# Kernel tuning notes

Measured on AMD Instinct MI355X. Metric: run time of the kernel, lower is better.

Reference implementation:

```python
import jax, jax.numpy as jnp
import numpy as np

N, E, R = 50000, 800000, 8
EMB, PROJ, H, OUT = 512, 256, 256, 200


def rgcn_conv(x, src, dst, rel, W, root, bias):
    # PyG RGCNConv: per-relation linear transform, mean aggregation per relation
    # over incoming edges, summed across relations, plus root transform + bias.
    n = x.shape[0]
    r, _, out_dim = W.shape
    h = jnp.einsum('ni,rio->nro', x, W)            # [N,R,out] per-relation transforms
    msgs = h[src, rel]                             # [E,out] gather per-edge messages
    seg = dst * r + rel                            # combined (node, relation) segment id
    sums = jax.ops.segment_sum(msgs, seg, num_segments=n * r)
    cnt = jax.ops.segment_sum(jnp.ones((src.shape[0],), x.dtype), seg, num_segments=n * r)
    mean = sums / jnp.maximum(cnt, 1.0)[:, None]
    agg = mean.reshape(n, r, out_dim).sum(axis=1)  # sum over relations
    return agg + x @ root + bias


def setup_inputs() -> dict:
    key = jax.random.key(0)
    ks = jax.random.split(key, 16)
    inp = {
        'embeddings': jax.random.normal(ks[0], (N, EMB), jnp.float32),
        'node_indices': jnp.arange(N, dtype=jnp.int64) if jax.config.jax_enable_x64 else jnp.arange(N, dtype=jnp.int32),
        'src': jax.random.randint(ks[1], (E,), 0, N),
        'dst': jax.random.randint(ks[2], (E,), 0, N),
        'rel': jax.random.randint(ks[3], (E,), 0, R),
        'neg_src': jax.random.randint(ks[4], (E,), 0, N),
        'neg_dst': jax.random.randint(ks[5], (E,), 0, N),
        'neg_rel': jax.random.randint(ks[6], (E,), 0, R),
        # learned parameters
        'Wp': jax.random.normal(ks[7], (EMB, PROJ), jnp.float32) * 0.04,
        'bp': jnp.zeros((PROJ,), jnp.float32),
        'W0': jax.random.normal(ks[8], (R, PROJ, H), jnp.float32) * 0.06,
        'root0': jax.random.normal(ks[9], (PROJ, H), jnp.float32) * 0.06,
        'b0': jnp.zeros((H,), jnp.float32),
        'W1': jax.random.normal(ks[10], (R, H, H), jnp.float32) * 0.06,
        'root1': jax.random.normal(ks[11], (H, H), jnp.float32) * 0.06,
        'b1': jnp.zeros((H,), jnp.float32),
        'W2': jax.random.normal(ks[12], (R, H, OUT), jnp.float32) * 0.06,
        'root2': jax.random.normal(ks[13], (H, OUT), jnp.float32) * 0.06,
        'b2': jnp.zeros((OUT,), jnp.float32),
        'rel_emb': jax.random.normal(ks[14], (R, OUT), jnp.float32),
    }
    return inp


def reference(embeddings, node_indices, src, dst, rel, neg_src, neg_dst, neg_rel,
              Wp, bp, W0, root0, b0, W1, root1, b1, W2, root2, b2, rel_emb):
    # projection: Linear per modality, then reorder rows by node index (sort)
    proj = embeddings @ Wp + bp                        # [N,PROJ]
    x = jnp.zeros_like(proj).at[node_indices].set(proj)
    # stacked RGCN encoder with relu between layers (no relu on last)
    x = jax.nn.relu(rgcn_conv(x, src, dst, rel, W0, root0, b0))
    x = jax.nn.relu(rgcn_conv(x, src, dst, rel, W1, root1, b1))
    out = rgcn_conv(x, src, dst, rel, W2, root2, b2)   # [N,OUT]
    # DistMult decoder over positive + negative triples
    s = jnp.concatenate([src, neg_src])
    o = jnp.concatenate([dst, neg_dst])
    r = jnp.concatenate([rel, neg_rel])
    scores = jnp.sum(out[s] * rel_emb[r] * out[o], axis=-1)  # [2E]
    return out, scores
```

## Files before the change

kernel.cpp:

```cpp
#include <hip/hip_runtime.h>
#include <stdint.h>

#define NN 50000
#define NE 800000
#define NR 8
#define EMBD 512
#define PROJD 256
#define HIDD 256
#define OUTD 200
#define NSEG (NN * NR)
#define CSR_CAP 1536

typedef _Float16 half8 __attribute__((ext_vector_type(8)));
typedef _Float16 half4 __attribute__((ext_vector_type(4)));
typedef float f32x4 __attribute__((ext_vector_type(4)));

__device__ __forceinline__ void gload16(const void* g, void* l) {
    __builtin_amdgcn_global_load_lds(
        reinterpret_cast<const __attribute__((address_space(1))) uint32_t*>(
            reinterpret_cast<uintptr_t>(g)),
        reinterpret_cast<__attribute__((address_space(3))) uint32_t*>(
            reinterpret_cast<uintptr_t>(l)),
        16, 0, 0);
}


__global__ void count_edges(const int* __restrict__ dst, const int* __restrict__ rel,
                            int* __restrict__ cnt, int E) {
    int e = blockIdx.x * 256 + threadIdx.x;
    if (e >= E) return;
    atomicAdd(&cnt[dst[e] * NR + rel[e]], 1);
}

__global__ __launch_bounds__(512) void scan1(const int* __restrict__ cnt, int* __restrict__ offs,
                                             int* __restrict__ bsums, int n) {
    __shared__ int sm[512];
    int tid = threadIdx.x;
    int g = blockIdx.x * 512 + tid;
    int v = (g < n) ? cnt[g] : 0;
    sm[tid] = v;
    __syncthreads();
    for (int o = 1; o < 512; o <<= 1) {
        int t = (tid >= o) ? sm[tid - o] : 0;
        __syncthreads();
        sm[tid] += t;
        __syncthreads();
    }
    if (g < n) offs[g] = sm[tid] - v;
    if (tid == 511) bsums[blockIdx.x] = sm[511];
}

__global__ __launch_bounds__(1024) void scan2(const int* __restrict__ bsums, int* __restrict__ bpref, int nb) {
    __shared__ int sm[1024];
    int tid = threadIdx.x;
    int v = (tid < nb) ? bsums[tid] : 0;
    sm[tid] = v;
    __syncthreads();
    for (int o = 1; o < 1024; o <<= 1) {
        int t = (tid >= o) ? sm[tid - o] : 0;
        __syncthreads();
        sm[tid] += t;
        __syncthreads();
    }
    if (tid < nb) bpref[tid] = sm[tid] - v;
}

__global__ __launch_bounds__(512) void scan3(int* __restrict__ offs, int* __restrict__ cursor,
                                             const int* __restrict__ bpref, int n, int total) {
    int g = blockIdx.x * 512 + threadIdx.x;
    if (g < n) {
        int v = offs[g] + bpref[blockIdx.x];
        offs[g] = v;
        cursor[g] = v;
    }
    if (g == 0) offs[n] = total;
}

__global__ void pad_offs(int* __restrict__ offs, int total) {
    offs[NSEG + 1 + blockIdx.x * 256 + threadIdx.x] = total;
}

__global__ void scatter_edges(const int* __restrict__ dst, const int* __restrict__ rel,
                              const int* __restrict__ src, int* __restrict__ cursor,
                              int* __restrict__ csr, int E) {
    int e = blockIdx.x * 256 + threadIdx.x;
    if (e >= E) return;
    int seg = dst[e] * NR + rel[e];
    int pos = atomicAdd(&cursor[seg], 1);
    csr[pos] = src[e];
}


__global__ void f32_to_f16_vec(const float* __restrict__ in, _Float16* __restrict__ out, long n4) {
    long i = (long)blockIdx.x * 256 + threadIdx.x;
    long stride = (long)gridDim.x * 256;
    for (; i < n4; i += stride) {
        float4 v = ((const float4*)in)[i];
        half4 h;
        h[0] = (_Float16)v.x; h[1] = (_Float16)v.y; h[2] = (_Float16)v.z; h[3] = (_Float16)v.w;
        ((half4*)out)[i] = h;
    }
}

__global__ void build_bt(const float* __restrict__ S0, int K0, const float* __restrict__ S1,
                         _Float16* __restrict__ Bt, int N, int K) {
    int k = blockIdx.x * 256 + threadIdx.x;
    int n = blockIdx.y;
    if (k >= K) return;
    float v = (k < K0) ? S0[(size_t)k * N + n] : S1[(size_t)(k - K0) * N + n];
    Bt[(size_t)n * K + k] = (_Float16)v;
}


template <bool RELU, bool LAST>
__global__ __launch_bounds__(512, 4) void rgcn_layer(
    const _Float16* __restrict__ x, const _Float16* __restrict__ Bt,
    const int* __restrict__ csr, const int* __restrict__ offs,
    const float* __restrict__ bias,
    _Float16* __restrict__ C16, int ldc, float* __restrict__ C32, int N) {
    __shared__ _Float16 As[64 * 256];
    __shared__ _Float16 Bs[2][256 * 32];
    __shared__ int offs_lds[520];
    __shared__ int csr_lds[CSR_CAP];
    const int tid = threadIdx.x;
    const int lane = tid & 63, wave = tid >> 6;
    const int lane32 = tid & 31, hw = tid >> 5;
    const int half_base = lane & 32;
    const int l15 = lane & 15, q = lane >> 4;
    const int wm = wave >> 2, wn = wave & 3;
    const int m0 = blockIdx.x * 64;
    const int segbase = m0 * NR;

    for (int i = tid; i < 513; i += 512) offs_lds[i] = offs[segbase + i];
    __syncthreads();
    const int e0 = offs_lds[0];
    const int e1 = offs_lds[512];
    const int ecnt = min(e1 - e0, CSR_CAP);
    for (int i = tid; i < ecnt; i += 512) csr_lds[i] = csr[e0 + i];
    __syncthreads();

    auto stage = [&](int buf, int g) {
        int kbase = g * 32;
#pragma unroll
        for (int h = 0; h < 2; ++h) {
            int s = tid + h * 512;
            int n = s >> 2, c4 = s & 3;
            int nn = n < N ? n : N - 1;
            gload16(Bt + (size_t)nn * 2304 + kbase + ((c4 ^ (n & 3)) << 3),
                    &Bs[buf][(size_t)(wave * 64 + h * 512) * 8]);
        }
    };

    f32x4 acc[2][4] = {};
    stage(0, 0);
    int cur = 0;
    for (int seg = 0; seg < 9; ++seg) {
#pragma unroll
        for (int u = 0; u < 4; ++u) {
            int lr = u * 16 + hw;
            int nd = m0 + lr;
            if (nd >= NN) nd = NN - 1;
            half8 hv;
            if (seg == 0) {
                hv = *(const half8*)(x + (size_t)nd * 256 + lane32 * 8);
            } else {
                int sb = lr * NR + seg - 1;
                int o0 = offs_lds[sb], o1 = offs_lds[sb + 1];
                int n = o1 - o0;
                if (n < 0) n = 0;
                if (n == 0) {
#pragma unroll
                    for (int z = 0; z < 8; ++z) hv[z] = (_Float16)0.f;
                } else {
                    bool staged = (o1 - e0) <= CSR_CAP;
                    int fi = o0 + (lane32 < n ? lane32 : n - 1);
                    int idxv = staged ? csr_lds[fi - e0] : csr[fi];
                    float a0=0.f,a1=0.f,a2=0.f,a3=0.f,a4=0.f,a5=0.f,a6=0.f,a7=0.f;
                    int nb = n < 32 ? n : 32;
                    int e = 0;
                    for (; e + 4 <= nb; e += 4) {
                        int s0 = __shfl(idxv, half_base + e);
                        int s1 = __shfl(idxv, half_base + e + 1);
                        int s2 = __shfl(idxv, half_base + e + 2);
                        int s3 = __shfl(idxv, half_base + e + 3);
                        half8 v0 = *(const half8*)(x + (size_t)s0 * 256 + lane32 * 8);
                        half8 v1 = *(const half8*)(x + (size_t)s1 * 256 + lane32 * 8);
                        half8 v2 = *(const half8*)(x + (size_t)s2 * 256 + lane32 * 8);
                        half8 v3 = *(const half8*)(x + (size_t)s3 * 256 + lane32 * 8);
                        a0 += ((float)v0[0] + (float)v1[0]) + ((float)v2[0] + (float)v3[0]);
                        a1 += ((float)v0[1] + (float)v1[1]) + ((float)v2[1] + (float)v3[1]);
                        a2 += ((float)v0[2] + (float)v1[2]) + ((float)v2[2] + (float)v3[2]);
                        a3 += ((float)v0[3] + (float)v1[3]) + ((float)v2[3] + (float)v3[3]);
                        a4 += ((float)v0[4] + (float)v1[4]) + ((float)v2[4] + (float)v3[4]);
                        a5 += ((float)v0[5] + (float)v1[5]) + ((float)v2[5] + (float)v3[5]);
                        a6 += ((float)v0[6] + (float)v1[6]) + ((float)v2[6] + (float)v3[6]);
                        a7 += ((float)v0[7] + (float)v1[7]) + ((float)v2[7] + (float)v3[7]);
                    }
                    for (; e < nb; ++e) {
                        int s0 = __shfl(idxv, half_base + e);
                        half8 v0 = *(const half8*)(x + (size_t)s0 * 256 + lane32 * 8);
                        a0 += (float)v0[0]; a1 += (float)v0[1];
                        a2 += (float)v0[2]; a3 += (float)v0[3];
                        a4 += (float)v0[4]; a5 += (float)v0[5];
                        a6 += (float)v0[6]; a7 += (float)v0[7];
                    }
                    for (int e2 = 32; e2 < n; ++e2) {
                        int s2i = staged ? csr_lds[o0 - e0 + e2] : csr[o0 + e2];
                        half8 v = *(const half8*)(x + (size_t)s2i * 256 + lane32 * 8);
                        a0 += (float)v[0]; a1 += (float)v[1];
                        a2 += (float)v[2]; a3 += (float)v[3];
                        a4 += (float)v[4]; a5 += (float)v[5];
                        a6 += (float)v[6]; a7 += (float)v[7];
                    }
                    float inv = 1.0f / (float)n;
                    hv[0] = (_Float16)(a0 * inv); hv[1] = (_Float16)(a1 * inv);
                    hv[2] = (_Float16)(a2 * inv); hv[3] = (_Float16)(a3 * inv);
                    hv[4] = (_Float16)(a4 * inv); hv[5] = (_Float16)(a5 * inv);
                    hv[6] = (_Float16)(a6 * inv); hv[7] = (_Float16)(a7 * inv);
                }
            }
            *(half8*)((char*)As + lr * 512 + ((lane32 ^ (lr & 31)) << 4)) = hv;
        }
        asm volatile("s_waitcnt lgkmcnt(0)" ::: "memory");
        __builtin_amdgcn_s_barrier();
        asm volatile("" ::: "memory");
        for (int ch = 0; ch < 8; ++ch) {
            int g = seg * 8 + ch;
            if (g < 71) {
                stage(cur ^ 1, g + 1);
                asm volatile("s_waitcnt vmcnt(2)" ::: "memory");
            } else {
                asm volatile("s_waitcnt vmcnt(0)" ::: "memory");
            }
            __builtin_amdgcn_s_barrier();
            asm volatile("" ::: "memory");
            half8 a[2], b[4];
#pragma unroll
            for (int i = 0; i < 2; ++i) {
                int row = wm * 32 + i * 16 + l15;
                int ck = ch * 4 + q;
                a[i] = *(const half8*)((const char*)As + row * 512 + ((ck ^ (row & 31)) << 4));
            }
#pragma unroll
            for (int j = 0; j < 4; ++j) {
                int n = wn * 64 + j * 16 + l15;
                b[j] = *(const half8*)((const char*)&Bs[cur][0] + n * 64 + ((q ^ (n & 3)) << 4));
            }
#pragma unroll
            for (int i = 0; i < 2; ++i)
#pragma unroll
                for (int j = 0; j < 4; ++j)
                    acc[i][j] = __builtin_amdgcn_mfma_f32_16x16x32_f16(a[i], b[j], acc[i][j], 0, 0, 0);
            asm volatile("s_waitcnt lgkmcnt(0)" ::: "memory");
            __builtin_amdgcn_s_barrier();
            asm volatile("" ::: "memory");
            cur ^= 1;
        }
    }
#pragma unroll
    for (int i = 0; i < 2; ++i) {
        int rbase = m0 + wm * 32 + i * 16 + q * 4;
#pragma unroll
        for (int j = 0; j < 4; ++j) {
            int cc = wn * 64 + j * 16 + l15;
            if (cc >= N) continue;
            float bv = bias[cc];
#pragma unroll
            for (int t = 0; t < 4; ++t) {
                int rr = rbase + t;
                if (rr >= NN) continue;
                float v = acc[i][j][t] + bv;
                if (RELU) v = fmaxf(v, 0.f);
                C16[(size_t)rr * ldc + cc] = (_Float16)v;
                if (LAST) C32[(size_t)rr * ldc + cc] = v;
            }
        }
    }
}


template <bool BIAS, bool ACC_IN, bool FINAL, bool RELU, bool LAST, bool SCATTER>
__global__ __launch_bounds__(256) void gemm16(
    const _Float16* __restrict__ A, int lda,
    const _Float16* __restrict__ Bt, int ldb,
    const float* __restrict__ bias, const int* __restrict__ sidx,
    _Float16* __restrict__ Cacc,
    _Float16* __restrict__ C16, int ldc, float* __restrict__ C32,
    int M, int N, int K) {
    __shared__ _Float16 As[2][4096];
    __shared__ _Float16 Bs[2][4096];
    const int tid = threadIdx.x;
    const int lane = tid & 63, wave = tid >> 6;
    const int wm = wave >> 1, wn = wave & 1;
    const int q = lane >> 4, l15 = lane & 15;
    const int m0 = blockIdx.y * 128, n0 = blockIdx.x * 128;
    const int wbase = wave * 512;
    f32x4 acc[4][4] = {};

    auto stage = [&](int buf, int k0) {
#pragma unroll
        for (int h = 0; h < 2; ++h) {
            int s = tid + h * 256;
            int r = s >> 2, c = s & 3;
            int cs = c ^ ((r >> 2) & 3);
            int ga = m0 + r; if (ga >= M) ga = M - 1;
            gload16(A + (size_t)ga * lda + k0 + cs * 8, &As[buf][wbase + h * 2048]);
            int gb = n0 + r; if (gb >= N) gb = N - 1;
            gload16(Bt + (size_t)gb * ldb + k0 + cs * 8, &Bs[buf][wbase + h * 2048]);
        }
    };

    const int nk = K >> 5;
    stage(0, 0);
    int cur = 0;
    for (int kt = 0; kt < nk; ++kt) {
        if (kt + 1 < nk) {
            stage(cur ^ 1, (kt + 1) << 5);
            asm volatile("s_waitcnt vmcnt(4)" ::: "memory");
        } else {
            asm volatile("s_waitcnt vmcnt(0)" ::: "memory");
        }
        __builtin_amdgcn_s_barrier();
        asm volatile("" ::: "memory");
        half8 a[4], b[4];
#pragma unroll
        for (int i = 0; i < 4; ++i) {
            int row = wm * 64 + i * 16 + l15;
            a[i] = *(const half8*)&As[cur][row * 32 + ((q ^ ((row >> 2) & 3)) << 3)];
            int col = wn * 64 + i * 16 + l15;
            b[i] = *(const half8*)&Bs[cur][col * 32 + ((q ^ ((col >> 2) & 3)) << 3)];
        }
#pragma unroll
        for (int i = 0; i < 4; ++i)
#pragma unroll
            for (int j = 0; j < 4; ++j)
                acc[i][j] = __builtin_amdgcn_mfma_f32_16x16x32_f16(a[i], b[j], acc[i][j], 0, 0, 0);
        asm volatile("s_waitcnt lgkmcnt(0)" ::: "memory");
        __builtin_amdgcn_s_barrier();
        asm volatile("" ::: "memory");
        cur ^= 1;
    }
#pragma unroll
    for (int i = 0; i < 4; ++i) {
        int rbase = m0 + wm * 64 + i * 16 + q * 4;
#pragma unroll
        for (int j = 0; j < 4; ++j) {
            int cc = n0 + wn * 64 + j * 16 + l15;
            if (cc >= N) continue;
#pragma unroll
            for (int t = 0; t < 4; ++t) {
                int rr = rbase + t;
                if (rr >= M) continue;
                float v = acc[i][j][t];
                if (BIAS) v += bias[cc];
                if (ACC_IN) v += (float)Cacc[(size_t)rr * 256 + cc];
                if (!FINAL) {
                    Cacc[(size_t)rr * 256 + cc] = (_Float16)v;
                } else {
                    if (RELU) v = fmaxf(v, 0.f);
                    int ro = SCATTER ? sidx[rr] : rr;
                    C16[(size_t)ro * ldc + cc] = (_Float16)v;
                    if (LAST) C32[(size_t)ro * ldc + cc] = v;
                }
            }
        }
    }
}


__global__ __launch_bounds__(256) void decoder16(
    const _Float16* __restrict__ out16, const _Float16* __restrict__ rel16,
    const int* __restrict__ src, const int* __restrict__ dst, const int* __restrict__ rel,
    const int* __restrict__ nsrc, const int* __restrict__ ndst, const int* __restrict__ nrel,
    float* __restrict__ scores) {
    int gid = blockIdx.x * 256 + threadIdx.x;
    int t = gid >> 3, lq = gid & 7;
    if (t >= 2 * NE) return;
    int s, o, r;
    if (t < NE) { s = src[t]; o = dst[t]; r = rel[t]; }
    else { int u = t - NE; s = nsrc[u]; o = ndst[u]; r = nrel[u]; }
    const half8* ps = (const half8*)(out16 + (size_t)s * OUTD);
    const half8* po = (const half8*)(out16 + (size_t)o * OUTD);
    const half8* pr = (const half8*)(rel16 + (size_t)r * OUTD);
    half8 hacc0 = {}, hacc1 = {};
#pragma unroll
    for (int it = 0; it < 4; ++it) {
        int c = it * 8 + lq;
        if (c < 25) {
            half8 a = ps[c], b = pr[c], d = po[c];
            half8 p = a * b * d;
            if (it & 1) hacc1 += p; else hacc0 += p;
        }
    }
    float acc = 0.f;
#pragma unroll
    for (int u = 0; u < 8; ++u) acc += (float)hacc0[u] + (float)hacc1[u];
#pragma unroll
    for (int off = 4; off; off >>= 1) acc += __shfl_xor(acc, off);
    if (lq == 0) scores[t] = acc;
}


extern "C" void kernel_launch(void* const* d_in, const int* in_sizes, int n_in,
                              void* d_out, int out_size, void* d_ws, size_t ws_size,
                              hipStream_t stream) {
    const float* emb   = (const float*)d_in[0];
    const int*   nidx  = (const int*)d_in[1];
    const int*   src   = (const int*)d_in[2];
    const int*   dst   = (const int*)d_in[3];
    const int*   rel   = (const int*)d_in[4];
    const int*   nsrc  = (const int*)d_in[5];
    const int*   ndst  = (const int*)d_in[6];
    const int*   nrel  = (const int*)d_in[7];
    const float* Wp    = (const float*)d_in[8];
    const float* bp    = (const float*)d_in[9];
    const float* W0    = (const float*)d_in[10];
    const float* root0 = (const float*)d_in[11];
    const float* b0    = (const float*)d_in[12];
    const float* W1    = (const float*)d_in[13];
    const float* root1 = (const float*)d_in[14];
    const float* b1    = (const float*)d_in[15];
    const float* W2    = (const float*)d_in[16];
    const float* root2 = (const float*)d_in[17];
    const float* b2    = (const float*)d_in[18];
    const float* rele  = (const float*)d_in[19];
    (void)in_sizes; (void)n_in; (void)out_size; (void)ws_size;

    float* out    = (float*)d_out;
    float* scores = out + (size_t)NN * OUTD;

    auto align = [](size_t x) { return (x + 255) & ~(size_t)255; };
    char* p = (char*)d_ws;
    auto alloc = [&](size_t bytes) -> char* {
        char* q = p; p += align(bytes); return q;
    };
    _Float16* emb16  = (_Float16*)alloc((size_t)NN * EMBD * 2);
    _Float16* xbufA  = (_Float16*)alloc((size_t)NN * 256 * 2);
    _Float16* xbufB  = (_Float16*)alloc((size_t)NN * 256 * 2);
    _Float16* out16  = xbufB;
    _Float16* Bt0 = (_Float16*)alloc((size_t)256 * 2304 * 2);
    _Float16* Bt1 = (_Float16*)alloc((size_t)256 * 2304 * 2);
    _Float16* Bt2 = (_Float16*)alloc((size_t)256 * 2304 * 2);
    _Float16* BtP = (_Float16*)alloc((size_t)256 * EMBD * 2);
    _Float16* rel16 = (_Float16*)alloc((size_t)NR * OUTD * 2);
    int*   cnt    = (int*)alloc((size_t)NSEG * 4);
    int*   cursor = (int*)alloc((size_t)NSEG * 4);
    int*   offs   = (int*)alloc((size_t)(NSEG + 1032) * 4);
    int*   csr    = (int*)alloc((size_t)NE * 4);
    int*   bsums  = (int*)alloc(4096);
    int*   bpref  = (int*)alloc(4096);

    hipMemsetAsync(cnt, 0, (size_t)NSEG * 4, stream);
    count_edges<<<(NE + 255) / 256, 256, 0, stream>>>(dst, rel, cnt, NE);
    const int NB = (NSEG + 511) / 512;
    scan1<<<NB, 512, 0, stream>>>(cnt, offs, bsums, NSEG);
    scan2<<<1, 1024, 0, stream>>>(bsums, bpref, NB);
    scan3<<<NB, 512, 0, stream>>>(offs, cursor, bpref, NSEG, NE);
    pad_offs<<<4, 256, 0, stream>>>(offs, NE);
    scatter_edges<<<(NE + 255) / 256, 256, 0, stream>>>(dst, rel, src, cursor, csr, NE);

    f32_to_f16_vec<<<2048, 256, 0, stream>>>(emb, emb16, (long)NN * EMBD / 4);
    f32_to_f16_vec<<<2, 256, 0, stream>>>(rele, rel16, (long)NR * OUTD / 4);
    build_bt<<<dim3(2, 256), 256, 0, stream>>>(Wp, EMBD, nullptr, BtP, PROJD, EMBD);
    build_bt<<<dim3(9, 256), 256, 0, stream>>>(root0, 256, W0, Bt0, HIDD, 2304);
    build_bt<<<dim3(9, 256), 256, 0, stream>>>(root1, 256, W1, Bt1, HIDD, 2304);
    build_bt<<<dim3(9, 200), 256, 0, stream>>>(root2, 256, W2, Bt2, OUTD, 2304);

    {
        dim3 g(2, (NN + 127) / 128);
        gemm16<true, false, true, false, false, true><<<g, 256, 0, stream>>>(
            emb16, EMBD, BtP, EMBD, bp, nidx, nullptr, xbufA, 256, nullptr, NN, 256, EMBD);
    }

    const int GL = (NN + 63) / 64;
    rgcn_layer<true, false><<<GL, 512, 0, stream>>>(xbufA, Bt0, csr, offs, b0,
                                                    xbufB, 256, nullptr, HIDD);
    rgcn_layer<true, false><<<GL, 512, 0, stream>>>(xbufB, Bt1, csr, offs, b1,
                                                    xbufA, 256, nullptr, HIDD);
    rgcn_layer<false, true><<<GL, 512, 0, stream>>>(xbufA, Bt2, csr, offs, b2,
                                                    out16, OUTD, out, OUTD);

    decoder16<<<(2 * NE * 8 + 255) / 256, 256, 0, stream>>>(out16, rel16, src, dst, rel,
                                                            nsrc, ndst, nrel, scores);
}
```

Measured before the change: 883.0 us.

## Give each wave private B column slices to drop per-chunk barriers in RGCN layer

Re-partitions the rgcn_layer MFMA tiling so each of the 8 waves owns a 32-column slice of the output across all 64 rows and stages only its own B rows into LDS. Because no wave reads another wave's B data, the two workgroup barriers per K-chunk are removed, leaving one barrier per segment. It also fully unrolls the chunk loop and raises wave priority around the MFMA block. Each wave now reads all four A fragments per chunk, which increases LDS read traffic. Separately, the pad_offs launch is folded into scan3 by running extra blocks that write the padding totals.

```diff
diff --git a/kernel.cpp b/kernel.cpp
--- a/kernel.cpp
+++ b/kernel.cpp
@@ -72,12 +72,9 @@
         int v = offs[g] + bpref[blockIdx.x];
         offs[g] = v;
         cursor[g] = v;
-    }
-    if (g == 0) offs[n] = total;
-}
-
-__global__ void pad_offs(int* __restrict__ offs, int total) {
-    offs[NSEG + 1 + blockIdx.x * 256 + threadIdx.x] = total;
+    } else if (g <= n + 1024) {
+        offs[g] = total;
+    }
 }
 
 __global__ void scatter_edges(const int* __restrict__ dst, const int* __restrict__ rel,
@@ -127,7 +124,6 @@
     const int lane32 = tid & 31, hw = tid >> 5;
     const int half_base = lane & 32;
     const int l15 = lane & 15, q = lane >> 4;
-    const int wm = wave >> 2, wn = wave & 3;
     const int m0 = blockIdx.x * 64;
     const int segbase = m0 * NR;
 
@@ -143,15 +139,16 @@
         int kbase = g * 32;
 #pragma unroll
         for (int h = 0; h < 2; ++h) {
-            int s = tid + h * 512;
-            int n = s >> 2, c4 = s & 3;
+            int s = lane + h * 64;
+            int n = wave * 32 + (s >> 2);
+            int c4 = s & 3;
             int nn = n < N ? n : N - 1;
             gload16(Bt + (size_t)nn * 2304 + kbase + ((c4 ^ (n & 3)) << 3),
-                    &Bs[buf][(size_t)(wave * 64 + h * 512) * 8]);
+                    &Bs[buf][wave * 1024 + h * 512]);
         }
     };
 
-    f32x4 acc[2][4] = {};
+    f32x4 acc[4][2] = {};
     stage(0, 0);
     int cur = 0;
     for (int seg = 0; seg < 9; ++seg) {
@@ -224,6 +221,7 @@
         asm volatile("s_waitcnt lgkmcnt(0)" ::: "memory");
         __builtin_amdgcn_s_barrier();
         asm volatile("" ::: "memory");
+#pragma unroll
         for (int ch = 0; ch < 8; ++ch) {
             int g = seg * 8 + ch;
             if (g < 71) {
@@ -232,39 +230,39 @@
             } else {
                 asm volatile("s_waitcnt vmcnt(0)" ::: "memory");
             }
-            __builtin_amdgcn_s_barrier();
-            asm volatile("" ::: "memory");
-            half8 a[2], b[4];
-#pragma unroll
-            for (int i = 0; i < 2; ++i) {
-                int row = wm * 32 + i * 16 + l15;
+            half8 a[4], b[2];
+#pragma unroll
+            for (int i = 0; i < 4; ++i) {
+                int row = i * 16 + l15;
                 int ck = ch * 4 + q;
                 a[i] = *(const half8*)((const char*)As + row * 512 + ((ck ^ (row & 31)) << 4));
             }
 #pragma unroll
-            for (int j = 0; j < 4; ++j) {
-                int n = wn * 64 + j * 16 + l15;
+            for (int j = 0; j < 2; ++j) {
+                int n = wave * 32 + j * 16 + l15;
                 b[j] = *(const half8*)((const char*)&Bs[cur][0] + n * 64 + ((q ^ (n & 3)) << 4));
             }
-#pragma unroll
-            for (int i = 0; i < 2; ++i)
-#pragma unroll
-                for (int j = 0; j < 4; ++j)
+            __builtin_amdgcn_s_setprio(1);
+#pragma unroll
+            for (int i = 0; i < 4; ++i)
+#pragma unroll
+                for (int j = 0; j < 2; ++j)
                     acc[i][j] = __builtin_amdgcn_mfma_f32_16x16x32_f16(a[i], b[j], acc[i][j], 0, 0, 0);
-            asm volatile("s_waitcnt lgkmcnt(0)" ::: "memory");
-            __builtin_amdgcn_s_barrier();
-            asm volatile("" ::: "memory");
+            __builtin_amdgcn_s_setprio(0);
             cur ^= 1;
         }
-    }
-#pragma unroll
-    for (int i = 0; i < 2; ++i) {
-        int rbase = m0 + wm * 32 + i * 16 + q * 4;
-#pragma unroll
-        for (int j = 0; j < 4; ++j) {
-            int cc = wn * 64 + j * 16 + l15;
-            if (cc >= N) continue;
-            float bv = bias[cc];
+        asm volatile("s_waitcnt lgkmcnt(0)" ::: "memory");
+        __builtin_amdgcn_s_barrier();
+        asm volatile("" ::: "memory");
+    }
+#pragma unroll
+    for (int j = 0; j < 2; ++j) {
+        int cc = wave * 32 + j * 16 + l15;
+        if (cc >= N) continue;
+        float bv = bias[cc];
+#pragma unroll
+        for (int i = 0; i < 4; ++i) {
+            int rbase = m0 + i * 16 + q * 4;
 #pragma unroll
             for (int t = 0; t < 4; ++t) {
                 int rr = rbase + t;
@@ -455,8 +453,7 @@
     const int NB = (NSEG + 511) / 512;
     scan1<<<NB, 512, 0, stream>>>(cnt, offs, bsums, NSEG);
     scan2<<<1, 1024, 0, stream>>>(bsums, bpref, NB);
-    scan3<<<NB, 512, 0, stream>>>(offs, cursor, bpref, NSEG, NE);
-    pad_offs<<<4, 256, 0, stream>>>(offs, NE);
+    scan3<<<NB + 3, 512, 0, stream>>>(offs, cursor, bpref, NSEG, NE);
     scatter_edges<<<(NE + 255) / 256, 256, 0, stream>>>(dst, rel, src, cursor, csr, NE);
 
     f32_to_f16_vec<<<2048, 256, 0, stream>>>(emb, emb16, (long)NN * EMBD / 4);
```

New measurement: 853.1 us. 1.04x faster.
